# Kernel tuning notes

Measured on AMD Instinct MI355X. Metric: run time of the kernel, lower is better.

## Reference

```python
import jax, jax.numpy as jnp
import numpy as np

DN = ('NCHW', 'OIHW', 'NCHW')


def conv2d(x, w, b, stride):
    y = jax.lax.conv_general_dilated(x, w, (stride, stride), 'VALID', dimension_numbers=DN)
    return y + b[None, :, None, None]


def split_heads(t, heads):
    # 'B (c h) H W -> B h (H W) c'  (channel index = c*heads + h)
    B, C, H, W = t.shape
    c = C // heads
    t = t.reshape(B, c, heads, H * W)
    return jnp.transpose(t, (0, 2, 3, 1))  # [B, h, HW, c]


def setup_inputs() -> dict:
    key = jax.random.key(0)
    ks = jax.random.split(key, 7)
    B, dim, H, W = 4, 256, 128, 128
    inner, p = 256, 8
    s = 0.02
    return {
        'x':  jax.random.normal(ks[0], (B, dim, H, W), jnp.float32),
        'Wq': jax.random.normal(ks[1], (inner, dim, 1, 1), jnp.float32) * s,
        'bq': jax.random.normal(ks[2], (inner,), jnp.float32) * s,
        'Wk': jax.random.normal(ks[3], (inner, dim, p, p), jnp.float32) * s,
        'bk': jax.random.normal(ks[4], (inner,), jnp.float32) * s,
        'Wv': jax.random.normal(ks[5], (inner, dim, p, p), jnp.float32) * s,
        'bv': jax.random.normal(ks[6], (inner,), jnp.float32) * s,
    }


def reference(x, Wq, bq, Wk, bk, Wv, bv):
    heads = 8
    p = Wk.shape[-1]
    B, C, H, W = x.shape
    q = conv2d(x, Wq, bq, 1)      # [B, inner, H, W]
    k = conv2d(x, Wk, bk, p)      # [B, inner, H/p, W/p]
    v = conv2d(x, Wv, bv, p)
    q = split_heads(q, heads)     # [B, h, HW, c]
    k = split_heads(k, heads)     # [B, h, K, c]
    v = split_heads(v, heads)
    # NOTE: original module applies no 1/sqrt(d) scaling
    dots = jnp.einsum('bhnc,bhkc->bhnk', q, k)
    attn = jax.nn.softmax(dots, axis=-1)
    out = jnp.einsum('bhnk,bhkc->bhnc', attn, v)  # [B, h, HW, c]
    # 'B h (H W) c -> B (c h) H W'
    c = out.shape[-1]
    out = jnp.transpose(out, (0, 3, 1, 2)).reshape(B, c * heads, H, W)
    return out
```

## Files before the change

### kernel.cpp

```cpp
#include <hip/hip_runtime.h>
#include <stdint.h>

typedef short sh4 __attribute__((ext_vector_type(4)));
typedef short short8 __attribute__((ext_vector_type(8)));
typedef float f32x4 __attribute__((ext_vector_type(4)));
typedef float f4 __attribute__((ext_vector_type(4)));
typedef _Float16 half4 __attribute__((ext_vector_type(4)));
typedef _Float16 half8 __attribute__((ext_vector_type(8)));
typedef unsigned int uint2v __attribute__((ext_vector_type(2)));

__device__ __forceinline__ short f2h(float f) {
    _Float16 h = (_Float16)f;
    return __builtin_bit_cast(short, h);
}

__device__ __forceinline__ f32x4 mfma_k32(short8 a, short8 b, f32x4 c) {
    return __builtin_amdgcn_mfma_f32_16x16x32_f16(
        __builtin_bit_cast(half8, a), __builtin_bit_cast(half8, b), c, 0, 0, 0);
}
__device__ __forceinline__ f32x4 mfma_k16(half4 a, half4 b, f32x4 c) {
    return __builtin_amdgcn_mfma_f32_16x16x16f16(a, b, c, 0, 0, 0);
}
__device__ __forceinline__ unsigned int pkrtz(float a, float b) {
    return __builtin_bit_cast(unsigned int, __builtin_amdgcn_cvt_pkrtz(a, b));
}
__device__ __forceinline__ float exp2_raw(float x) {
    float r;
    asm("v_exp_f32 %0, %1" : "=v"(r) : "v"(x));
    return r;
}


__device__ __forceinline__ void transpose64(const float* __restrict__ src,
                                            short* __restrict__ dst,
                                            int srcSlowStride, int dstRowStride,
                                            float (*tile)[65]) {
    const int t = threadIdx.x;
#pragma unroll
    for (int i = 0; i < 4; ++i) {
        int idx = i * 1024 + t * 4;
        int fast = idx & 63, slow = idx >> 6;
        f4 v = *(const f4*)(src + (long)slow * srcSlowStride + fast);
        tile[slow][fast]     = v[0];
        tile[slow][fast + 1] = v[1];
        tile[slow][fast + 2] = v[2];
        tile[slow][fast + 3] = v[3];
    }
    __syncthreads();
#pragma unroll
    for (int i = 0; i < 2; ++i) {
        int ch = i * 256 + t;
        int fast = ch >> 3, sg = ch & 7;
        short8 v;
#pragma unroll
        for (int j = 0; j < 8; ++j) v[j] = f2h(tile[sg * 8 + j][fast]);
        *(short8*)(dst + (long)fast * dstRowStride + sg * 8) = v;
    }
}

__global__ __launch_bounds__(256) void k_pack_all(const float* __restrict__ x,
                                                  const float* __restrict__ wk,
                                                  const float* __restrict__ wv,
                                                  const float* __restrict__ wq,
                                                  short* __restrict__ xn,
                                                  short* __restrict__ wp,
                                                  short* __restrict__ wqp) {
    __shared__ float tile[64][65];
    int bid = blockIdx.x;
    if (bid < 4096) {
        int bi = bid;
        int ct = bi & 3, pxt = (bi >> 2) & 255, b = bi >> 10;
        const float* src = x + (((long)(b * 256 + ct * 64)) << 14) + (long)pxt * 64;
        short* dst = xn + (((long)(b << 14) + pxt * 64) * 256) + ct * 64;
        transpose64(src, dst, 16384, 256, tile);
    } else if (bid < 6144) {
        int bi = bid - 4096;
        int ct = bi & 3, oc = bi >> 2;
        const float* base = (oc < 256) ? (wk + (long)oc * 16384)
                                       : (wv + (long)(oc - 256) * 16384);
        const float* src = base + ct * 4096;
        short* dst = wp + (long)oc * 16384 + ct * 64;
        transpose64(src, dst, 64, 256, tile);
    } else {
        int i = (bid - 6144) * 256 + threadIdx.x;
        wqp[i] = f2h(wq[i]);
    }
}


__device__ __forceinline__ void kv_gemm_body(const short* __restrict__ xn,
                                             const short* __restrict__ wp,
                                             float* __restrict__ part,
                                             int bid, short* smem) {
    short* Al = smem;
    short* Bl = smem + 8192;
    int wg = (bid & 7) * 64 + (bid >> 3);
    int nb = wg & 7, pm = (wg >> 3) & 7, kc = wg >> 6;
    int t = threadIdx.x, l = t & 63, w = t >> 6;
    int wm = w >> 1, wn = w & 1;
    int low = l & 15, q = l >> 4;

    short* lda[4];
    short* ldb[2];
#pragma unroll
    for (int i = 0; i < 4; ++i) {
        int g = i * 256 + t;
        int row = g >> 3, lg = g & 7;
        lda[i] = Al + row * 64 + ((lg ^ (row & 7)) * 8);
    }
#pragma unroll
    for (int i = 0; i < 2; ++i) {
        int g = i * 256 + t;
        int row = g >> 3, lg = g & 7;
        ldb[i] = Bl + row * 64 + ((lg ^ (row & 7)) * 8);
    }

    f32x4 acc[4][2];
#pragma unroll
    for (int mt = 0; mt < 4; ++mt)
#pragma unroll
        for (int nt = 0; nt < 2; ++nt) acc[mt][nt] = (f32x4){0.f, 0.f, 0.f, 0.f};

#pragma unroll 1
    for (int kk4 = 0; kk4 < 8; ++kk4) {
        const short* apt[4];
        const short* bpt[2];
        int dydx = kc * 8 + kk4;
#pragma unroll
        for (int i = 0; i < 4; ++i) {
            int g = i * 256 + t;
            int row = g >> 3, lg = g & 7;
            int patch = pm * 128 + row;
            int bb = patch >> 8, pid = patch & 255;
            int ph = pid >> 4, pw = pid & 15;
            int px = (ph * 8 + (dydx >> 3)) * 128 + pw * 8 + (dydx & 7);
            apt[i] = xn + ((long)(bb << 14) + px) * 256 + lg * 8;
        }
#pragma unroll
        for (int i = 0; i < 2; ++i) {
            int g = i * 256 + t;
            int row = g >> 3, lg = g & 7;
            int oc = nb * 64 + row;
            bpt[i] = wp + (long)oc * 16384 + kc * 2048 + kk4 * 256 + lg * 8;
        }
#pragma unroll
        for (int j = 0; j < 4; ++j) {
            short8 va[4], vb[2];
#pragma unroll
            for (int i = 0; i < 4; ++i) va[i] = *(const short8*)(apt[i] + j * 64);
#pragma unroll
            for (int i = 0; i < 2; ++i) vb[i] = *(const short8*)(bpt[i] + j * 64);
#pragma unroll
            for (int i = 0; i < 4; ++i) *(short8*)lda[i] = va[i];
#pragma unroll
            for (int i = 0; i < 2; ++i) *(short8*)ldb[i] = vb[i];
            __syncthreads();
#pragma unroll
            for (int ks = 0; ks < 2; ++ks) {
                short8 af[4], bf[2];
#pragma unroll
                for (int mt = 0; mt < 4; ++mt) {
                    int row = wm * 64 + mt * 16 + low;
                    int lg = ks * 4 + q;
                    af[mt] = *(const short8*)(Al + row * 64 + ((lg ^ (row & 7)) * 8));
                }
#pragma unroll
                for (int nt = 0; nt < 2; ++nt) {
                    int row = wn * 32 + nt * 16 + low;
                    int lg = ks * 4 + q;
                    bf[nt] = *(const short8*)(Bl + row * 64 + ((lg ^ (row & 7)) * 8));
                }
#pragma unroll
                for (int mt = 0; mt < 4; ++mt)
#pragma unroll
                    for (int nt = 0; nt < 2; ++nt)
                        acc[mt][nt] = mfma_k32(af[mt], bf[nt], acc[mt][nt]);
            }
            __syncthreads();
        }
    }
#pragma unroll
    for (int mt = 0; mt < 4; ++mt) {
        int patch = pm * 128 + wm * 64 + mt * 16 + q * 4;
#pragma unroll
        for (int nt = 0; nt < 2; ++nt) {
            int oc = nb * 64 + wn * 32 + nt * 16 + low;
#pragma unroll
            for (int r = 0; r < 4; ++r)
                part[((long)kc * 1024 + patch + r) * 512 + oc] = acc[mt][nt][r];
        }
    }
}

__device__ __forceinline__ void q_gemm_body(const short* __restrict__ xn,
                                            const short* __restrict__ wqp,
                                            const float* __restrict__ bq,
                                            short* __restrict__ qp,
                                            int bi, short* smem) {
    short* Tb = smem;
    int b = bi >> 8, tile = bi & 255;
    long px0 = (long)tile * 64;
    int t = threadIdx.x, l = t & 63, w = t >> 6;
    int low = l & 15, q = l >> 4;

    const short* xb = xn + (((long)(b << 14)) + px0) * 256;

    float bqv[4];
#pragma unroll
    for (int nt = 0; nt < 4; ++nt) bqv[nt] = bq[w * 64 + nt * 16 + low];

    f32x4 acc[4][4];
#pragma unroll
    for (int mt = 0; mt < 4; ++mt)
#pragma unroll
        for (int nt = 0; nt < 4; ++nt) acc[mt][nt] = (f32x4){0.f, 0.f, 0.f, 0.f};

#pragma unroll
    for (int kstep = 0; kstep < 8; ++kstep) {
        short8 af[4], bf[4];
#pragma unroll
        for (int mt = 0; mt < 4; ++mt)
            af[mt] = *(const short8*)(xb + (mt * 16 + low) * 256 + kstep * 32 + q * 8);
#pragma unroll
        for (int nt = 0; nt < 4; ++nt)
            bf[nt] = *(const short8*)(wqp + (w * 64 + nt * 16 + low) * 256 + kstep * 32 + q * 8);
#pragma unroll
        for (int mt = 0; mt < 4; ++mt)
#pragma unroll
            for (int nt = 0; nt < 4; ++nt)
                acc[mt][nt] = mfma_k32(af[mt], bf[nt], acc[mt][nt]);
    }
    const float LOG2E = 1.44269504088896f;
#pragma unroll
    for (int mt = 0; mt < 4; ++mt)
#pragma unroll
        for (int nt = 0; nt < 4; ++nt) {
            int oc = w * 64 + nt * 16 + low;
            int h8 = oc & 7, cc = oc >> 3;
            int gi = h8 * 4 + (cc >> 3);
#pragma unroll
            for (int r = 0; r < 4; ++r) {
                int px = mt * 16 + q * 4 + r;
                Tb[px * 256 + ((gi ^ (px & 7)) * 8) + (cc & 7)] =
                    f2h((acc[mt][nt][r] + bqv[nt]) * LOG2E);
            }
        }
    __syncthreads();
#pragma unroll
    for (int i = 0; i < 8; ++i) {
        int g = i * 256 + t;
        int pxl = g >> 5, g16 = g & 31;
        int hh = g16 >> 2, oct = g16 & 3;
        short8 v = *(const short8*)(Tb + pxl * 256 + ((g16 ^ (pxl & 7)) * 8));
        *(short8*)(qp + (((long)(b * 8 + hh) * 16384) + px0 + pxl) * 32 + oct * 8) = v;
    }
}

__global__ __launch_bounds__(256) void k_gemm_all(const short* __restrict__ xn,
                                                  const short* __restrict__ wp,
                                                  const short* __restrict__ wqp,
                                                  const float* __restrict__ bq,
                                                  float* __restrict__ part,
                                                  short* __restrict__ qp) {
    __shared__ __attribute__((aligned(16))) short smem[16384];
    int bid = blockIdx.x;
    int k3 = bid / 3, r3 = bid - k3 * 3;
    if (r3 == 2) kv_gemm_body(xn, wp, part, k3, smem);
    else         q_gemm_body(xn, wqp, bq, qp, k3 * 2 + r3, smem);
}

__global__ __launch_bounds__(256) void k_kv_fin(const float* __restrict__ part,
                                                const float* __restrict__ bk,
                                                const float* __restrict__ bv,
                                                short* __restrict__ kp,
                                                short* __restrict__ vp) {
    int idx = blockIdx.x * 256 + threadIdx.x;
    int oc = idx & 511, patch = idx >> 9;
    float s = 0.f;
#pragma unroll
    for (int kc = 0; kc < 8; ++kc) s += part[(long)kc * 524288 + idx];
    int b = patch >> 8, key = patch & 255;
    if (oc < 256) {
        s += bk[oc];
        kp[(((long)(b * 8 + (oc & 7)) * 256) + key) * 32 + (oc >> 3)] = f2h(s);
    } else {
        int o = oc - 256;
        s += bv[o];
        vp[(((long)(b * 8 + (o & 7)) * 32) + (o >> 3)) * 256 + key] = f2h(s);
    }
}

__global__ __launch_bounds__(256) void k_attn(const short* __restrict__ qp,
                                              const short* __restrict__ kp,
                                              const short* __restrict__ vp,
                                              float* __restrict__ out) {
    __shared__ short Vl[32 * 264];
    int bi = blockIdx.x;
    int tile = bi & 63, h = (bi >> 6) & 7, b = bi >> 9;
    int bh = b * 8 + h;
    long px0 = (long)tile * 256;
    int t = threadIdx.x, l = t & 63, w = t >> 6;
    int low = l & 15, q = l >> 4;

    const short* kbase = kp + (long)bh * 8192;
    const short* vbase = vp + (long)bh * 8192;
    const short* qbase = qp + (long)bh * 16384 * 32;

#pragma unroll
    for (int i = 0; i < 4; ++i) {
        int g = i * 256 + t;
        int c = g >> 5, k8 = g & 31;
        *(short8*)(Vl + c * 264 + k8 * 8) = *(const short8*)(vbase + c * 256 + k8 * 8);
    }
    short8 kf[16];
#pragma unroll
    for (int mt = 0; mt < 16; ++mt)
        kf[mt] = *(const short8*)(kbase + (mt * 16 + low) * 32 + q * 8);
    __syncthreads();

    const short* vA = Vl + low * 264 + q * 4;
    const sh4 sone = {0x3C00, 0x3C00, 0x3C00, 0x3C00};
    const half4 vones = __builtin_bit_cast(half4, sone);

#pragma unroll 1
    for (int nt = 0; nt < 4; ++nt) {
        long px = px0 + w * 64 + nt * 16 + low;
        short8 bq2 = *(const short8*)(qbase + px * 32 + q * 8);

        f32x4 dd[16];
        float m = -1e30f;
#pragma unroll
        for (int mt = 0; mt < 16; ++mt) {
            dd[mt] = mfma_k32(kf[mt], bq2, (f32x4){0.f, 0.f, 0.f, 0.f});
            m = fmaxf(fmaxf(dd[mt][0], dd[mt][1]), m);
            m = fmaxf(fmaxf(dd[mt][2], dd[mt][3]), m);
        }
        m = fmaxf(m, __shfl_xor(m, 16));
        m = fmaxf(m, __shfl_xor(m, 32));

        uint2v pk[16];
#pragma unroll
        for (int mt = 0; mt < 16; ++mt) {
            float p0 = exp2_raw(dd[mt][0] - m);
            float p1 = exp2_raw(dd[mt][1] - m);
            float p2 = exp2_raw(dd[mt][2] - m);
            float p3 = exp2_raw(dd[mt][3] - m);
            pk[mt][0] = pkrtz(p0, p1);
            pk[mt][1] = pkrtz(p2, p3);
        }

        f32x4 o2[2], os;
        o2[0] = (f32x4){0.f, 0.f, 0.f, 0.f};
        o2[1] = (f32x4){0.f, 0.f, 0.f, 0.f};
        os    = (f32x4){0.f, 0.f, 0.f, 0.f};
        __builtin_amdgcn_s_setprio(1);
#pragma unroll
        for (int kc = 0; kc < 16; ++kc) {
            half4 pb = __builtin_bit_cast(half4, pk[kc]);
            half4 av0 = __builtin_bit_cast(half4, *(const sh4*)(vA + kc * 16));
            half4 av1 = __builtin_bit_cast(half4, *(const sh4*)(vA + 4224 + kc * 16));
            o2[0] = mfma_k16(av0, pb, o2[0]);
            o2[1] = mfma_k16(av1, pb, o2[1]);
            os    = mfma_k16(vones, pb, os);
        }
        __builtin_amdgcn_s_setprio(0);
        float inv = 1.0f / os[0];

#pragma unroll
        for (int ct = 0; ct < 2; ++ct)
#pragma unroll
            for (int r = 0; r < 4; ++r) {
                int c = ct * 16 + q * 4 + r;
                out[(((long)(b * 256 + c * 8 + h)) << 14) + px] = o2[ct][r] * inv;
            }
    }
}

extern "C" void kernel_launch(void* const* d_in, const int* in_sizes, int n_in,
                              void* d_out, int out_size, void* d_ws, size_t ws_size,
                              hipStream_t stream) {
    const float* x  = (const float*)d_in[0];
    const float* Wq = (const float*)d_in[1];
    const float* bq = (const float*)d_in[2];
    const float* Wk = (const float*)d_in[3];
    const float* bk = (const float*)d_in[4];
    const float* Wv = (const float*)d_in[5];
    const float* bv = (const float*)d_in[6];
    float* out = (float*)d_out;

    char* ws = (char*)d_ws;
    const size_t OFF_XN = 0;
    const size_t OFF_Q  = 33554432;
    const size_t OFF_WP = 67108864;
    const size_t OFF_WQ = 83886080;
    const size_t OFF_KP = 84017152;
    const size_t OFF_VP = 84541440;
    const size_t OFF_PT = 85065728;
    const size_t NEEDED = 118620160;
    if (ws_size < NEEDED) return;

    short* xn  = (short*)(ws + OFF_XN);
    short* qp  = (short*)(ws + OFF_Q);
    short* wp  = (short*)(ws + OFF_WP);
    short* wqp = (short*)(ws + OFF_WQ);
    short* kp  = (short*)(ws + OFF_KP);
    short* vp  = (short*)(ws + OFF_VP);
    float* part= (float*)(ws + OFF_PT);

    k_pack_all<<<dim3(6400), dim3(256), 0, stream>>>(x, Wk, Wv, Wq, xn, wp, wqp);
    k_gemm_all<<<dim3(1536), dim3(256), 0, stream>>>(xn, wp, wqp, bq, part, qp);
    k_kv_fin  <<<dim3(2048), dim3(256), 0, stream>>>(part, bk, bv, kp, vp);
    k_attn    <<<dim3(2048), dim3(256), 0, stream>>>(qp, kp, vp, out);
}
```

Before: 150.2 us.

## Split fused Q/KV GEMM kernel and shrink KV GEMM tile to 64 patches

Replaces the combined k_gemm_all kernel, which interleaved Q-projection and KV-conv blocks, with two separate kernels. The KV GEMM moves from 128-patch to 64-patch tiles, doubling its block count to 1024 and cutting LDS use per block. The Q GEMM launches after the KV finalize. This adds a kernel launch and a serialization point, and gives up the co-scheduling of the two GEMMs in exchange for more KV parallelism and smaller LDS footprints.

```diff
diff --git a/kernel.cpp b/kernel.cpp
--- a/kernel.cpp
+++ b/kernel.cpp
@@ -87,50 +87,44 @@
     }
 }
 
-
-__device__ __forceinline__ void kv_gemm_body(const short* __restrict__ xn,
-                                             const short* __restrict__ wp,
-                                             float* __restrict__ part,
-                                             int bid, short* smem) {
-    short* Al = smem;
-    short* Bl = smem + 8192;
-    int wg = (bid & 7) * 64 + (bid >> 3);
-    int nb = wg & 7, pm = (wg >> 3) & 7, kc = wg >> 6;
+__global__ __launch_bounds__(256) void k_kv_gemm(const short* __restrict__ xn,
+                                                 const short* __restrict__ wp,
+                                                 float* __restrict__ part) {
+    __shared__ short Al[64 * 64];
+    __shared__ short Bl[64 * 64];
+    int bid = blockIdx.x;
+    int wg = (bid & 7) * 128 + (bid >> 3);
+    int nb = wg & 7, pm = (wg >> 3) & 15, kc = wg >> 7;
     int t = threadIdx.x, l = t & 63, w = t >> 6;
     int wm = w >> 1, wn = w & 1;
     int low = l & 15, q = l >> 4;
 
-    short* lda[4];
+    short* lda[2];
     short* ldb[2];
 #pragma unroll
-    for (int i = 0; i < 4; ++i) {
+    for (int i = 0; i < 2; ++i) {
         int g = i * 256 + t;
         int row = g >> 3, lg = g & 7;
         lda[i] = Al + row * 64 + ((lg ^ (row & 7)) * 8);
-    }
-#pragma unroll
-    for (int i = 0; i < 2; ++i) {
-        int g = i * 256 + t;
-        int row = g >> 3, lg = g & 7;
         ldb[i] = Bl + row * 64 + ((lg ^ (row & 7)) * 8);
     }
 
-    f32x4 acc[4][2];
-#pragma unroll
-    for (int mt = 0; mt < 4; ++mt)
+    f32x4 acc[2][2];
+#pragma unroll
+    for (int mt = 0; mt < 2; ++mt)
 #pragma unroll
         for (int nt = 0; nt < 2; ++nt) acc[mt][nt] = (f32x4){0.f, 0.f, 0.f, 0.f};
 
 #pragma unroll 1
     for (int kk4 = 0; kk4 < 8; ++kk4) {
-        const short* apt[4];
+        const short* apt[2];
         const short* bpt[2];
         int dydx = kc * 8 + kk4;
 #pragma unroll
-        for (int i = 0; i < 4; ++i) {
+        for (int i = 0; i < 2; ++i) {
             int g = i * 256 + t;
             int row = g >> 3, lg = g & 7;
-            int patch = pm * 128 + row;
+            int patch = pm * 64 + row;
             int bb = patch >> 8, pid = patch & 255;
             int ph = pid >> 4, pw = pid & 15;
             int px = (ph * 8 + (dydx >> 3)) * 128 + pw * 8 + (dydx & 7);
@@ -145,22 +139,22 @@
         }
 #pragma unroll
         for (int j = 0; j < 4; ++j) {
-            short8 va[4], vb[2];
-#pragma unroll
-            for (int i = 0; i < 4; ++i) va[i] = *(const short8*)(apt[i] + j * 64);
+            short8 va[2], vb[2];
+#pragma unroll
+            for (int i = 0; i < 2; ++i) va[i] = *(const short8*)(apt[i] + j * 64);
 #pragma unroll
             for (int i = 0; i < 2; ++i) vb[i] = *(const short8*)(bpt[i] + j * 64);
 #pragma unroll
-            for (int i = 0; i < 4; ++i) *(short8*)lda[i] = va[i];
+            for (int i = 0; i < 2; ++i) *(short8*)lda[i] = va[i];
 #pragma unroll
             for (int i = 0; i < 2; ++i) *(short8*)ldb[i] = vb[i];
             __syncthreads();
 #pragma unroll
             for (int ks = 0; ks < 2; ++ks) {
-                short8 af[4], bf[2];
-#pragma unroll
-                for (int mt = 0; mt < 4; ++mt) {
-                    int row = wm * 64 + mt * 16 + low;
+                short8 af[2], bf[2];
+#pragma unroll
+                for (int mt = 0; mt < 2; ++mt) {
+                    int row = wm * 32 + mt * 16 + low;
                     int lg = ks * 4 + q;
                     af[mt] = *(const short8*)(Al + row * 64 + ((lg ^ (row & 7)) * 8));
                 }
@@ -171,7 +165,7 @@
                     bf[nt] = *(const short8*)(Bl + row * 64 + ((lg ^ (row & 7)) * 8));
                 }
 #pragma unroll
-                for (int mt = 0; mt < 4; ++mt)
+                for (int mt = 0; mt < 2; ++mt)
 #pragma unroll
                     for (int nt = 0; nt < 2; ++nt)
                         acc[mt][nt] = mfma_k32(af[mt], bf[nt], acc[mt][nt]);
@@ -180,8 +174,8 @@
         }
     }
 #pragma unroll
-    for (int mt = 0; mt < 4; ++mt) {
-        int patch = pm * 128 + wm * 64 + mt * 16 + q * 4;
+    for (int mt = 0; mt < 2; ++mt) {
+        int patch = pm * 64 + wm * 32 + mt * 16 + q * 4;
 #pragma unroll
         for (int nt = 0; nt < 2; ++nt) {
             int oc = nb * 64 + wn * 32 + nt * 16 + low;
@@ -190,83 +184,6 @@
                 part[((long)kc * 1024 + patch + r) * 512 + oc] = acc[mt][nt][r];
         }
     }
-}
-
-__device__ __forceinline__ void q_gemm_body(const short* __restrict__ xn,
-                                            const short* __restrict__ wqp,
-                                            const float* __restrict__ bq,
-                                            short* __restrict__ qp,
-                                            int bi, short* smem) {
-    short* Tb = smem;
-    int b = bi >> 8, tile = bi & 255;
-    long px0 = (long)tile * 64;
-    int t = threadIdx.x, l = t & 63, w = t >> 6;
-    int low = l & 15, q = l >> 4;
-
-    const short* xb = xn + (((long)(b << 14)) + px0) * 256;
-
-    float bqv[4];
-#pragma unroll
-    for (int nt = 0; nt < 4; ++nt) bqv[nt] = bq[w * 64 + nt * 16 + low];
-
-    f32x4 acc[4][4];
-#pragma unroll
-    for (int mt = 0; mt < 4; ++mt)
-#pragma unroll
-        for (int nt = 0; nt < 4; ++nt) acc[mt][nt] = (f32x4){0.f, 0.f, 0.f, 0.f};
-
-#pragma unroll
-    for (int kstep = 0; kstep < 8; ++kstep) {
-        short8 af[4], bf[4];
-#pragma unroll
-        for (int mt = 0; mt < 4; ++mt)
-            af[mt] = *(const short8*)(xb + (mt * 16 + low) * 256 + kstep * 32 + q * 8);
-#pragma unroll
-        for (int nt = 0; nt < 4; ++nt)
-            bf[nt] = *(const short8*)(wqp + (w * 64 + nt * 16 + low) * 256 + kstep * 32 + q * 8);
-#pragma unroll
-        for (int mt = 0; mt < 4; ++mt)
-#pragma unroll
-            for (int nt = 0; nt < 4; ++nt)
-                acc[mt][nt] = mfma_k32(af[mt], bf[nt], acc[mt][nt]);
-    }
-    const float LOG2E = 1.44269504088896f;
-#pragma unroll
-    for (int mt = 0; mt < 4; ++mt)
-#pragma unroll
-        for (int nt = 0; nt < 4; ++nt) {
-            int oc = w * 64 + nt * 16 + low;
-            int h8 = oc & 7, cc = oc >> 3;
-            int gi = h8 * 4 + (cc >> 3);
-#pragma unroll
-            for (int r = 0; r < 4; ++r) {
-                int px = mt * 16 + q * 4 + r;
-                Tb[px * 256 + ((gi ^ (px & 7)) * 8) + (cc & 7)] =
-                    f2h((acc[mt][nt][r] + bqv[nt]) * LOG2E);
-            }
-        }
-    __syncthreads();
-#pragma unroll
-    for (int i = 0; i < 8; ++i) {
-        int g = i * 256 + t;
-        int pxl = g >> 5, g16 = g & 31;
-        int hh = g16 >> 2, oct = g16 & 3;
-        short8 v = *(const short8*)(Tb + pxl * 256 + ((g16 ^ (pxl & 7)) * 8));
-        *(short8*)(qp + (((long)(b * 8 + hh) * 16384) + px0 + pxl) * 32 + oct * 8) = v;
-    }
-}
-
-__global__ __launch_bounds__(256) void k_gemm_all(const short* __restrict__ xn,
-                                                  const short* __restrict__ wp,
-                                                  const short* __restrict__ wqp,
-                                                  const float* __restrict__ bq,
-                                                  float* __restrict__ part,
-                                                  short* __restrict__ qp) {
-    __shared__ __attribute__((aligned(16))) short smem[16384];
-    int bid = blockIdx.x;
-    int k3 = bid / 3, r3 = bid - k3 * 3;
-    if (r3 == 2) kv_gemm_body(xn, wp, part, k3, smem);
-    else         q_gemm_body(xn, wqp, bq, qp, k3 * 2 + r3, smem);
 }
 
 __global__ __launch_bounds__(256) void k_kv_fin(const float* __restrict__ part,
@@ -287,6 +204,70 @@
         int o = oc - 256;
         s += bv[o];
         vp[(((long)(b * 8 + (o & 7)) * 32) + (o >> 3)) * 256 + key] = f2h(s);
+    }
+}
+
+__global__ __launch_bounds__(256) void k_q_gemm(const short* __restrict__ xn,
+                                                const short* __restrict__ wqp,
+                                                const float* __restrict__ bq,
+                                                short* __restrict__ qp) {
+    __shared__ short Tb[64 * 256];
+    int bi = blockIdx.x;
+    int b = bi >> 8, tile = bi & 255;
+    long px0 = (long)tile * 64;
+    int t = threadIdx.x, l = t & 63, w = t >> 6;
+    int low = l & 15, q = l >> 4;
+
+    const short* xb = xn + (((long)(b << 14)) + px0) * 256;
+
+    float bqv[4];
+#pragma unroll
+    for (int nt = 0; nt < 4; ++nt) bqv[nt] = bq[w * 64 + nt * 16 + low];
+
+    f32x4 acc[4][4];
+#pragma unroll
+    for (int mt = 0; mt < 4; ++mt)
+#pragma unroll
+        for (int nt = 0; nt < 4; ++nt) acc[mt][nt] = (f32x4){0.f, 0.f, 0.f, 0.f};
+
+#pragma unroll
+    for (int kstep = 0; kstep < 8; ++kstep) {
+        short8 af[4], bf[4];
+#pragma unroll
+        for (int mt = 0; mt < 4; ++mt)
+            af[mt] = *(const short8*)(xb + (mt * 16 + low) * 256 + kstep * 32 + q * 8);
+#pragma unroll
+        for (int nt = 0; nt < 4; ++nt)
+            bf[nt] = *(const short8*)(wqp + (w * 64 + nt * 16 + low) * 256 + kstep * 32 + q * 8);
+#pragma unroll
+        for (int mt = 0; mt < 4; ++mt)
+#pragma unroll
+            for (int nt = 0; nt < 4; ++nt)
+                acc[mt][nt] = mfma_k32(af[mt], bf[nt], acc[mt][nt]);
+    }
+    const float LOG2E = 1.44269504088896f;
+#pragma unroll
+    for (int mt = 0; mt < 4; ++mt)
+#pragma unroll
+        for (int nt = 0; nt < 4; ++nt) {
+            int oc = w * 64 + nt * 16 + low;
+            int h8 = oc & 7, cc = oc >> 3;
+            int gi = h8 * 4 + (cc >> 3);
+#pragma unroll
+            for (int r = 0; r < 4; ++r) {
+                int px = mt * 16 + q * 4 + r;
+                Tb[px * 256 + ((gi ^ (px & 7)) * 8) + (cc & 7)] =
+                    f2h((acc[mt][nt][r] + bqv[nt]) * LOG2E);
+            }
+        }
+    __syncthreads();
+#pragma unroll
+    for (int i = 0; i < 8; ++i) {
+        int g = i * 256 + t;
+        int pxl = g >> 5, g16 = g & 31;
+        int hh = g16 >> 2, oct = g16 & 3;
+        short8 v = *(const short8*)(Tb + pxl * 256 + ((g16 ^ (pxl & 7)) * 8));
+        *(short8*)(qp + (((long)(b * 8 + hh) * 16384) + px0 + pxl) * 32 + oct * 8) = v;
     }
 }
 
@@ -408,7 +389,8 @@
     float* part= (float*)(ws + OFF_PT);
 
     k_pack_all<<<dim3(6400), dim3(256), 0, stream>>>(x, Wk, Wv, Wq, xn, wp, wqp);
-    k_gemm_all<<<dim3(1536), dim3(256), 0, stream>>>(xn, wp, wqp, bq, part, qp);
+    k_kv_gemm <<<dim3(1024), dim3(256), 0, stream>>>(xn, wp, part);
     k_kv_fin  <<<dim3(2048), dim3(256), 0, stream>>>(part, bk, bv, kp, vp);
+    k_q_gemm  <<<dim3(1024), dim3(256), 0, stream>>>(xn, wqp, bq, qp);
     k_attn    <<<dim3(2048), dim3(256), 0, stream>>>(qp, kp, vp, out);
 }
```

Result: faster. 142.2 us, median of 2 (-5.3%).
